# Kernel tuning notes

Hardware: AMD Instinct MI355X
Metric: run time of the kernel (lower is better)

Reference implementation:

```python
import jax, jax.numpy as jnp
import numpy as np
import math

T, R, H, DK = 3, 4, 8, 32   # num_types, num_relations, n_heads, d_k
OUT = H * DK                # out_dim = 256
IN = 256                    # in_dim (== out_dim, required by residual)
B, N = 4, 1024              # batch, max_nodes
LN_EPS = 1e-5


def setup_inputs() -> dict:
    key = jax.random.key(0)
    ks = jax.random.split(key, 12)
    a = math.sqrt(6.0 / (2 * DK))  # xavier_uniform bound for [d_k,d_k]
    w = 0.02
    return {
        "node_features":   jax.random.normal(ks[0], (B, N, IN), jnp.float32),
        "node_types_soft": jax.random.uniform(ks[1], (B, N, T), jnp.float32),
        "adj_matrix_soft": jax.random.uniform(ks[2], (B, N, N), jnp.float32),
        "edge_types_soft": jax.random.uniform(ks[3], (B, N, N, R), jnp.float32),
        "Wq": jax.random.normal(ks[4], (T, IN, OUT), jnp.float32) * w,
        "bq": jnp.zeros((T, OUT), jnp.float32),
        "Wk": jax.random.normal(ks[5], (T, IN, OUT), jnp.float32) * w,
        "bk": jnp.zeros((T, OUT), jnp.float32),
        "Wv": jax.random.normal(ks[6], (T, IN, OUT), jnp.float32) * w,
        "bv": jnp.zeros((T, OUT), jnp.float32),
        "Wa": jax.random.normal(ks[7], (T, OUT, OUT), jnp.float32) * w,
        "ba": jnp.zeros((T, OUT), jnp.float32),
        "rel_pri": jnp.ones((R, H), jnp.float32),
        "rel_att": jax.random.uniform(ks[8], (R, H, DK, DK), jnp.float32, -a, a),
        "rel_msg": jax.random.uniform(ks[9], (R, H, DK, DK), jnp.float32, -a, a),
        "skip": jnp.ones((T,), jnp.float32),
        "ln_gamma": jnp.ones((T, OUT), jnp.float32),
        "ln_beta": jnp.zeros((T, OUT), jnp.float32),
    }


def _single(x, types, adj, erel, Wq, bq, Wk, bk, Wv, bv, Wa, ba,
            rel_pri, rel_att, rel_msg, skip, ln_gamma, ln_beta):
    # x:[N,in], types:[N,T], adj:[N,N], erel:[N,N,R]
    n = x.shape[0]
    sqrt_dk = float(np.sqrt(DK))
    # per-type projections -> [T,N,H,DK]
    Qt = (jnp.einsum('nd,tdo->tno', x, Wq) + bq[:, None, :]).reshape(T, n, H, DK)
    Kt = (jnp.einsum('nd,tdo->tno', x, Wk) + bk[:, None, :]).reshape(T, n, H, DK)
    Vt = (jnp.einsum('nd,tdo->tno', x, Wv) + bv[:, None, :]).reshape(T, n, H, DK)
    # relation-transformed K/V: [T,R,N,H,DK]
    Ksr = jnp.einsum('tnhd,rhde->trnhe', Kt, rel_att)
    Vsr = jnp.einsum('tnhd,rhde->trnhe', Vt, rel_msg)
    # soft-type mixtures (sums over target/source types factor out of the mask)
    Qbar = jnp.einsum('nt,tnhd->nhd', types, Qt)            # target mix
    Kbar = jnp.einsum('nt,trnhd->rnhd', types, Ksr)         # source mix, per relation
    # accumulated (masked, unnormalized) attention logits [N,N,H]
    res_att = jnp.zeros((n, n, H), x.dtype)
    for r in range(R):
        coef = (adj * erel[:, :, r])[:, :, None] * (rel_pri[r] / sqrt_dk)  # [N,N,H]
        res_att = res_att + coef * jnp.einsum('ihd,jhd->ijh', Qbar, Kbar[r])
    # per-target-row softmax over sources (dim j), zeroed if row-sum tiny
    row_sum = res_att.sum(axis=(1, 2))                       # [N]
    attn = jnp.where((row_sum > 1e-6)[:, None, None],
                     jax.nn.softmax(res_att, axis=1), 0.0)
    # aggregated = sum_{s,r,j} attn * masked score * V_{s,r}  (never builds [N,N,H,DK])
    agg = jnp.zeros((n, H, DK), x.dtype)
    for r in range(R):
        coef = (adj * erel[:, :, r])[:, :, None] * (rel_pri[r] / sqrt_dk)
        for s in range(T):
            score = coef * types[None, :, s, None] * jnp.einsum('ihd,jhd->ijh', Qbar, Ksr[s, r])
            agg = agg + jnp.einsum('ijh,ijh,jhd->ihd', attn, score, Vsr[s, r])
    agg = agg.reshape(n, OUT)
    # per-type output head: a_linear(gelu(agg)), gated residual, layernorm, soft-type mix
    g = jax.nn.gelu(agg, approximate=False)
    trans = jnp.einsum('no,tod->tnd', g, Wa) + ba[:, None, :]          # [T,N,OUT]
    alpha = jax.nn.sigmoid(skip)[:, None, None]
    res = trans * alpha + x[None] * (1.0 - alpha)
    mu = res.mean(axis=-1, keepdims=True)
    var = ((res - mu) ** 2).mean(axis=-1, keepdims=True)
    ln = (res - mu) / jnp.sqrt(var + LN_EPS) * ln_gamma[:, None, :] + ln_beta[:, None, :]
    return jnp.einsum('nt,tnd->nd', types, ln)


def reference(node_features, node_types_soft, adj_matrix_soft, edge_types_soft,
              Wq, bq, Wk, bk, Wv, bv, Wa, ba, rel_pri, rel_att, rel_msg,
              skip, ln_gamma, ln_beta):
    f = jax.vmap(_single, in_axes=(0, 0, 0, 0) + (None,) * 14)
    return f(node_features, node_types_soft, adj_matrix_soft, edge_types_soft,
             Wq, bq, Wk, bk, Wv, bv, Wa, ba, rel_pri, rel_att, rel_msg,
             skip, ln_gamma, ln_beta)
```

## Files before the change

kernel.cpp:

```cpp
#include <hip/hip_runtime.h>
#include <math.h>

constexpr int CB = 4, CN = 1024, CT = 3, CR = 4, CH = 8, CDK = 32, COUT = 256;

typedef __attribute__((ext_vector_type(4))) float f32x4;
typedef __attribute__((ext_vector_type(8))) short s16x8;
typedef __attribute__((ext_vector_type(2))) _Float16 f16x2;
typedef __attribute__((ext_vector_type(4))) _Float16 f16x4;
typedef __attribute__((ext_vector_type(8))) _Float16 f16x8;
typedef __attribute__((ext_vector_type(4))) unsigned short u16x4;
typedef __attribute__((ext_vector_type(8))) unsigned short u16x8;

union W4 { f16x4 v4; f16x2 v2[2]; };

__device__ inline unsigned short f2bf(float x) {
    unsigned u = __float_as_uint(x);
    unsigned r = (u + 0x7fffu + ((u >> 16) & 1u)) >> 16;
    return (unsigned short)r;
}
__device__ inline float bf2f(unsigned short b) {
    return __uint_as_float(((unsigned)b) << 16);
}
__device__ inline f16x2 pk2(float a, float b) {
    auto t = __builtin_amdgcn_cvt_pkrtz(a, b);
    f16x2 r;
    __builtin_memcpy(&r, &t, sizeof(r));
    return r;
}

__global__ __launch_bounds__(256) void prep0(
    const float* __restrict__ nf,
    unsigned short* __restrict__ Xh, unsigned short* __restrict__ Xl,
    const float* __restrict__ Wq, const float* __restrict__ Wk,
    const float* __restrict__ Wv, const float* __restrict__ Wa,
    unsigned short* __restrict__ WTh, unsigned short* __restrict__ WTl,
    const float* __restrict__ rel_msg, _Float16* __restrict__ MT,
    float* __restrict__ rs,
    const float* __restrict__ adj, const float* __restrict__ erel,
    float* __restrict__ coefT)
{
    __shared__ float smem[32 * 132];
    const int bx = blockIdx.x, tid = threadIdx.x;
    if (bx < 1024) {
        size_t idx = ((size_t)bx * 256 + tid) * 4;
        f32x4 v = *(const f32x4*)(nf + idx);
        u16x4 hv, lv;
        #pragma unroll
        for (int k = 0; k < 4; ++k) {
            unsigned short hb = f2bf(v[k]);
            hv[k] = hb; lv[k] = f2bf(v[k] - bf2f(hb));
        }
        *(u16x4*)(Xh + idx) = hv;
        *(u16x4*)(Xl + idx) = lv;
    } else if (bx < 1792) {
        int w = bx - 1024;
        int zz = w >> 6; int rem = w & 63;
        int k0 = (rem >> 3) * 32, n0 = (rem & 7) * 32;
        int t = zz % 3;
        const float* W;
        if (zz < 9) { int w3 = zz / 3; W = (w3 == 0 ? Wq : (w3 == 1 ? Wk : Wv)); }
        else W = Wa;
        W += (size_t)t * COUT * COUT;
        {
            int k = tid >> 3, n4 = (tid & 7) * 4;
            f32x4 v = *(const f32x4*)(W + (size_t)(k0 + k) * COUT + n0 + n4);
            smem[(n4 + 0) * 33 + k] = v[0]; smem[(n4 + 1) * 33 + k] = v[1];
            smem[(n4 + 2) * 33 + k] = v[2]; smem[(n4 + 3) * 33 + k] = v[3];
        }
        __syncthreads();
        int n = tid >> 3, k4 = (tid & 7) * 4;
        u16x4 hv, lv;
        #pragma unroll
        for (int j = 0; j < 4; ++j) {
            float x = smem[n * 33 + k4 + j];
            unsigned short hb = f2bf(x);
            hv[j] = hb; lv[j] = f2bf(x - bf2f(hb));
        }
        size_t off = (size_t)zz * COUT * COUT + (size_t)(n0 + n) * COUT + k0 + k4;
        *(u16x4*)(WTh + off) = hv;
        *(u16x4*)(WTl + off) = lv;
    } else if (bx < 1824) {
        int rh = bx - 1792;
        int e = tid >> 3, ep4 = (tid & 7) * 4;
        f16x4 o;
        #pragma unroll
        for (int k = 0; k < 4; ++k)
            o[k] = (_Float16)rel_msg[((size_t)rh * 32 + ep4 + k) * 32 + e];
        *(f16x4*)(MT + ((size_t)rh * 32 + e) * 32 + ep4) = o;
    } else if (bx < 1840) {
        rs[(bx - 1824) * 256 + tid] = 0.f;
    } else {
        int c = bx - 1840;
        int b = c >> 10; int rem = c & 1023;
        int i0 = (rem >> 5) * 32; int j0 = (rem & 31) * 32;
        {
            int ii = tid >> 3, jc = tid & 7;
            size_t arow = ((size_t)b * CN + i0 + ii) * CN + j0;
            f32x4 av = *(const f32x4*)(adj + arow + jc * 4);
            #pragma unroll
            for (int kk = 0; kk < 4; ++kk) {
                int j = jc * 4 + kk;
                f32x4 ev = *(const f32x4*)(erel + (arow + j) * 4);
                float a = av[kk];
                f32x4 cv;
                cv[0] = ev[0] * a; cv[1] = ev[1] * a; cv[2] = ev[2] * a; cv[3] = ev[3] * a;
                *(f32x4*)&smem[j * 132 + ii * 4] = cv;
            }
        }
        __syncthreads();
        {
            int jj = tid >> 3, ic = tid & 7;
            size_t orow = ((size_t)b * CN + j0 + jj) * CN + i0;
            #pragma unroll
            for (int kk = 0; kk < 4; ++kk)
                *(f32x4*)(coefT + (orow + ic * 4 + kk) * 4) =
                    *(const f32x4*)&smem[jj * 132 + (ic * 4 + kk) * 4];
        }
    }
}

__global__ __launch_bounds__(256) void mfma_gemm(
    int mode,
    const unsigned short* __restrict__ Ah, const unsigned short* __restrict__ Al,
    const unsigned short* __restrict__ WTh, const unsigned short* __restrict__ WTl,
    const float* __restrict__ bq, const float* __restrict__ bk,
    const float* __restrict__ bv, const float* __restrict__ ba,
    float* __restrict__ Y0, float* __restrict__ Y1, float* __restrict__ Y2)
{
    int z = blockIdx.z;
    int b, t, widx;
    const float* bias;
    float* Y;
    if (mode == 0) {
        b = z / 9; int r9 = z % 9; int w3 = r9 / 3; t = r9 % 3;
        widx = w3 * 3 + t;
        bias = (w3 == 0 ? bq : (w3 == 1 ? bk : bv)) + t * COUT;
        Y = (w3 == 0 ? Y0 : (w3 == 1 ? Y1 : Y2)) + ((size_t)b * CT + t) * CN * COUT;
    } else {
        b = z / CT; t = z % CT;
        widx = 9 + t;
        bias = ba + t * COUT;
        Y = Y0 + ((size_t)b * CT + t) * CN * COUT;
    }
    const unsigned short* Ahb = Ah + (size_t)b * CN * COUT;
    const unsigned short* Alb = Al + (size_t)b * CN * COUT;
    const unsigned short* Bhb = WTh + (size_t)widx * COUT * COUT;
    const unsigned short* Blb = WTl + (size_t)widx * COUT * COUT;

    const int M0 = blockIdx.x * 128, N0 = blockIdx.y * 128;
    __shared__ unsigned short As[2][128][40];
    __shared__ unsigned short Bs[2][128][40];
    const int tid = threadIdx.x;
    const int wave = tid >> 6, lane = tid & 63;
    const int wm = wave & 1, wn = wave >> 1;
    const int col = lane & 15, quad = lane >> 4;

    f32x4 acc[4][4];
    #pragma unroll
    for (int mt = 0; mt < 4; ++mt)
        #pragma unroll
        for (int nt = 0; nt < 4; ++nt) acc[mt][nt] = (f32x4){0.f, 0.f, 0.f, 0.f};

    for (int kt = 0; kt < COUT; kt += 32) {
        #pragma unroll
        for (int q = 0; q < 2; ++q) {
            int f = q * 256 + tid;
            int m = f >> 2, kc = (f & 3) * 8;
            *(u16x8*)&As[0][m][kc] = *(const u16x8*)(Ahb + (size_t)(M0 + m) * COUT + kt + kc);
            *(u16x8*)&As[1][m][kc] = *(const u16x8*)(Alb + (size_t)(M0 + m) * COUT + kt + kc);
            *(u16x8*)&Bs[0][m][kc] = *(const u16x8*)(Bhb + (size_t)(N0 + m) * COUT + kt + kc);
            *(u16x8*)&Bs[1][m][kc] = *(const u16x8*)(Blb + (size_t)(N0 + m) * COUT + kt + kc);
        }
        __syncthreads();
        s16x8 ah[4], al4[4], bh[4], bl4[4];
        #pragma unroll
        for (int mt = 0; mt < 4; ++mt) {
            ah[mt]  = *(const s16x8*)&As[0][wm * 64 + mt * 16 + col][quad * 8];
            al4[mt] = *(const s16x8*)&As[1][wm * 64 + mt * 16 + col][quad * 8];
        }
        #pragma unroll
        for (int nt = 0; nt < 4; ++nt) {
            bh[nt]  = *(const s16x8*)&Bs[0][wn * 64 + nt * 16 + col][quad * 8];
            bl4[nt] = *(const s16x8*)&Bs[1][wn * 64 + nt * 16 + col][quad * 8];
        }
        #pragma unroll
        for (int mt = 0; mt < 4; ++mt)
            #pragma unroll
            for (int nt = 0; nt < 4; ++nt) {
                acc[mt][nt] = __builtin_amdgcn_mfma_f32_16x16x32_bf16(al4[mt], bh[nt], acc[mt][nt], 0, 0, 0);
                acc[mt][nt] = __builtin_amdgcn_mfma_f32_16x16x32_bf16(ah[mt], bl4[nt], acc[mt][nt], 0, 0, 0);
                acc[mt][nt] = __builtin_amdgcn_mfma_f32_16x16x32_bf16(ah[mt], bh[nt], acc[mt][nt], 0, 0, 0);
            }
        __syncthreads();
    }
    float bb[4];
    #pragma unroll
    for (int nt = 0; nt < 4; ++nt) bb[nt] = bias[N0 + wn * 64 + nt * 16 + col];
    #pragma unroll
    for (int mt = 0; mt < 4; ++mt)
        #pragma unroll
        for (int nt = 0; nt < 4; ++nt) {
            int n = N0 + wn * 64 + nt * 16 + col;
            #pragma unroll
            for (int reg = 0; reg < 4; ++reg) {
                int m = M0 + wm * 64 + mt * 16 + quad * 4 + reg;
                Y[(size_t)m * COUT + n] = acc[mt][nt][reg] + bb[nt];
            }
        }
}

__global__ void mix_qbar(const float* __restrict__ Qt, const float* __restrict__ types,
                         float* __restrict__ Qbar)
{
    int idx = blockIdx.x * 256 + threadIdx.x;
    int bi = idx >> 6;
    int o4 = (idx & 63) * 4;
    int b = bi >> 10;
    const float* tp = types + (size_t)bi * CT;
    float t0 = tp[0], t1 = tp[1], t2 = tp[2];
    size_t nbase = ((size_t)b * CT) * CN * COUT + (size_t)(bi & 1023) * COUT + o4;
    float4 q0 = *(const float4*)(Qt + nbase);
    float4 q1 = *(const float4*)(Qt + nbase + (size_t)CN * COUT);
    float4 q2 = *(const float4*)(Qt + nbase + 2 * (size_t)CN * COUT);
    float4 o;
    o.x = t0 * q0.x + t1 * q1.x + t2 * q2.x;
    o.y = t0 * q0.y + t1 * q1.y + t2 * q2.y;
    o.z = t0 * q0.z + t1 * q1.z + t2 * q2.z;
    o.w = t0 * q0.w + t1 * q1.w + t2 * q2.w;
    *(float4*)(Qbar + (size_t)bi * COUT + o4) = o;
}

__global__ __launch_bounds__(256) void qr3_kernel(const float* __restrict__ Qbar,
                                                  const float* __restrict__ rel_att,
                                                  const float* __restrict__ rel_pri,
                                                  unsigned short* __restrict__ Qrhi,
                                                  unsigned short* __restrict__ Qrlo)
{
    int i0 = blockIdx.x * 8;
    int rh = blockIdx.y; int r = rh >> 3, h = rh & 7;
    int b = blockIdx.z;
    __shared__ float A_s[32][33];
    __shared__ float q_s[8][32];
    int tid = threadIdx.x;
    {
        int f = tid * 4; int d = f >> 5, e = f & 31;
        float4 v = *(const float4*)(rel_att + ((size_t)rh * 32 + d) * 32 + e);
        A_s[d][e] = v.x; A_s[d][e + 1] = v.y; A_s[d][e + 2] = v.z; A_s[d][e + 3] = v.w;
        int ii = tid >> 5, ee = tid & 31;
        q_s[ii][ee] = Qbar[((size_t)b * CN + i0 + ii) * COUT + h * CDK + ee];
    }
    __syncthreads();
    int d = tid & 31, ii = tid >> 5;
    float acc = 0.f;
    #pragma unroll 8
    for (int e = 0; e < 32; ++e) acc += A_s[d][e] * q_s[ii][e];
    const float inv_sqrt = 0.17677669529663687f;
    float v = acc * rel_pri[rh] * inv_sqrt;
    unsigned short hb = f2bf(v);
    float lo = v - bf2f(hb);
    size_t oidx = ((((size_t)b * CR + r) * CH + h) * CN + i0 + ii) * CDK + d;
    Qrhi[oidx] = hb;
    Qrlo[oidx] = f2bf(lo);
}

__global__ __launch_bounds__(256) void prep_kv(
    const float* __restrict__ Kt, const float* __restrict__ Vt,
    const float* __restrict__ types,
    unsigned short* __restrict__ Kbh, unsigned short* __restrict__ Kbl,
    unsigned short* __restrict__ Kty, _Float16* __restrict__ VT)
{
    __shared__ float tile[32][72];
    const int bx = blockIdx.x, tid = threadIdx.x;
    if (bx < 512) {
        int b = bx >> 7, jt = bx & 127;
        int j = jt * 8 + (tid >> 5);
        int c = tid & 31;
        int h = c >> 2, d0 = (c & 3) * 8;
        const float* tp = types + ((size_t)b * CN + j) * CT;
        float kb[8];
        #pragma unroll
        for (int k = 0; k < 8; ++k) kb[k] = 0.f;
        #pragma unroll
        for (int s = 0; s < 3; ++s) {
            float ty = tp[s];
            const float* src = Kt + (((size_t)(b * 3 + s)) * CN + j) * COUT + c * 8;
            f32x4 a0 = *(const f32x4*)(src);
            f32x4 a1 = *(const f32x4*)(src + 4);
            u16x8 kt8;
            #pragma unroll
            for (int k = 0; k < 4; ++k) {
                float v0 = ty * a0[k], v1 = ty * a1[k];
                kt8[k] = f2bf(v0); kt8[4 + k] = f2bf(v1);
                kb[k] += v0; kb[4 + k] += v1;
            }
            *(u16x8*)(Kty + (((size_t)(b * 3 + s) * CH + h) * CN + j) * CDK + d0) = kt8;
        }
        u16x8 hv, lv;
        #pragma unroll
        for (int k = 0; k < 8; ++k) {
            unsigned short hb = f2bf(kb[k]);
            hv[k] = hb; lv[k] = f2bf(kb[k] - bf2f(hb));
        }
        *(u16x8*)(Kbh + (((size_t)b * CH + h) * CN + j) * CDK + d0) = hv;
        *(u16x8*)(Kbl + (((size_t)b * CH + h) * CN + j) * CDK + d0) = lv;
    } else {
        int idx2 = bx - 512;
        int bs = idx2 >> 7; int rem = idx2 & 127;
        int h = rem >> 4; int j0 = (rem & 15) * 64;
        int jj = tid >> 2, e8 = (tid & 3) * 8;
        const float* src = Vt + ((size_t)bs * CN + j0 + jj) * COUT + h * CDK + e8;
        f32x4 v0 = *(const f32x4*)(src);
        f32x4 v1 = *(const f32x4*)(src + 4);
        #pragma unroll
        for (int k = 0; k < 4; ++k) { tile[e8 + k][jj] = v0[k]; tile[e8 + 4 + k][jj] = v1[k]; }
        __syncthreads();
        int e = tid >> 3, jr = (tid & 7) * 8;
        f16x8 o;
        #pragma unroll
        for (int k = 0; k < 8; ++k) o[k] = (_Float16)tile[e][jr + k];
        int jg = j0 + jr;
        int js = jg >> 4, jp = jg & 15;
        *(f16x8*)(VT + ((size_t)(bs * CH + h) * 64 + js) * 512 + e * 16 + jp) = o;
    }
}

__global__ __launch_bounds__(256, 3) void attn5_kernel(
    const unsigned short* __restrict__ Qrhi, const unsigned short* __restrict__ Qrlo,
    const unsigned short* __restrict__ Kbh,  const unsigned short* __restrict__ Kbl,
    const unsigned short* __restrict__ Kty,
    const _Float16* __restrict__ VT,
    const float* __restrict__ coefT,
    float* __restrict__ Upart, float* __restrict__ lbuf, float* __restrict__ rowsum)
{
    const int h = blockIdx.y;
    const int z = blockIdx.z; const int b = z >> 1, part = z & 1;
    const int tid = threadIdx.x;
    const int wave = tid >> 6, lane = tid & 63;
    const int col = lane & 15, quad = lane >> 4;
    const int i = blockIdx.x * 64 + wave * 16 + col;
    const int jbase = part * 512;

    s16x8 qh[4], ql[4];
    #pragma unroll
    for (int r = 0; r < 4; ++r) {
        size_t off = ((((size_t)b * CR + r) * CH + h) * CN + i) * CDK + quad * 8;
        qh[r] = *(const s16x8*)(Qrhi + off);
        ql[r] = *(const s16x8*)(Qrlo + off);
    }

    f32x4 U[4][2];
    #pragma unroll
    for (int r = 0; r < 4; ++r) { U[r][0] = (f32x4){0.f,0.f,0.f,0.f}; U[r][1] = (f32x4){0.f,0.f,0.f,0.f}; }
    float lpart = 0.f, rspart = 0.f;

    const size_t kbbase = (((size_t)b * CH + h) * CN + col) * CDK + quad * 8;
    size_t ktbase[3];
    #pragma unroll
    for (int s = 0; s < 3; ++s)
        ktbase[s] = (((size_t)(b * 3 + s) * CH + h) * CN + col) * CDK + quad * 8;
    const size_t cfrow = ((size_t)b * CN + quad * 4) * CN + i;
    size_t vb[3];
    #pragma unroll
    for (int s = 0; s < 3; ++s)
        vb[s] = ((size_t)((b * 3 + s) * CH + h) * 64) * 512 + col * 16 + quad * 4;

    s16x8 p_bh[2], p_bl[2];
    f32x4 p_cf[2][4];
    f16x4 p_v0[2][3], p_v1[2][3];
    {
        const int j0 = jbase;
        p_bh[0] = *(const s16x8*)(Kbh + kbbase + (size_t)j0 * CDK);
        p_bl[0] = *(const s16x8*)(Kbl + kbbase + (size_t)j0 * CDK);
        #pragma unroll
        for (int reg = 0; reg < 4; ++reg)
            p_cf[0][reg] = *(const f32x4*)(coefT + (cfrow + (size_t)(j0 + reg) * CN) * 4);
        const size_t vo = (size_t)(j0 >> 4) * 512;
        #pragma unroll
        for (int s = 0; s < 3; ++s) {
            p_v0[0][s] = *(const f16x4*)(VT + vb[s] + vo);
            p_v1[0][s] = *(const f16x4*)(VT + vb[s] + vo + 256);
        }
    }

    #pragma unroll 2
    for (int js = 0; js < 32; ++js) {
        const int cur = js & 1, nx = cur ^ 1;
        const int j0 = jbase + js * 16;
        s16x8 kt0 = *(const s16x8*)(Kty + ktbase[0] + (size_t)j0 * CDK);
        s16x8 kt1 = *(const s16x8*)(Kty + ktbase[1] + (size_t)j0 * CDK);
        s16x8 kt2 = *(const s16x8*)(Kty + ktbase[2] + (size_t)j0 * CDK);
        const int jn = jbase + ((js + 1 < 32) ? (js + 1) * 16 : js * 16);
        p_bh[nx] = *(const s16x8*)(Kbh + kbbase + (size_t)jn * CDK);
        p_bl[nx] = *(const s16x8*)(Kbl + kbbase + (size_t)jn * CDK);
        #pragma unroll
        for (int reg = 0; reg < 4; ++reg)
            p_cf[nx][reg] = *(const f32x4*)(coefT + (cfrow + (size_t)(jn + reg) * CN) * 4);
        const size_t von = (size_t)(jn >> 4) * 512;
        #pragma unroll
        for (int s = 0; s < 3; ++s) {
            p_v0[nx][s] = *(const f16x4*)(VT + vb[s] + von);
            p_v1[nx][s] = *(const f16x4*)(VT + vb[s] + von + 256);
        }

        f32x4 Db[4];
        #pragma unroll
        for (int r = 0; r < 4; ++r) {
            f32x4 d = {0.f, 0.f, 0.f, 0.f};
            d = __builtin_amdgcn_mfma_f32_16x16x32_bf16(p_bl[cur], qh[r], d, 0, 0, 0);
            d = __builtin_amdgcn_mfma_f32_16x16x32_bf16(p_bh[cur], ql[r], d, 0, 0, 0);
            d = __builtin_amdgcn_mfma_f32_16x16x32_bf16(p_bh[cur], qh[r], d, 0, 0, 0);
            Db[r] = d;
        }
        float P[4];
        #pragma unroll
        for (int reg = 0; reg < 4; ++reg) {
            float L = p_cf[cur][reg][0] * Db[0][reg] + p_cf[cur][reg][1] * Db[1][reg]
                    + p_cf[cur][reg][2] * Db[2][reg] + p_cf[cur][reg][3] * Db[3][reg];
            rspart += L;
            P[reg] = __expf(L);
            lpart += P[reg];
        }
        f16x2 pA[4], pB[4];
        #pragma unroll
        for (int r = 0; r < 4; ++r) {
            pA[r] = pk2(P[0] * p_cf[cur][0][r], P[1] * p_cf[cur][1][r]);
            pB[r] = pk2(P[2] * p_cf[cur][2][r], P[3] * p_cf[cur][3][r]);
        }
        #pragma unroll
        for (int s = 0; s < 3; ++s) {
            s16x8 kts = (s == 0) ? kt0 : (s == 1) ? kt1 : kt2;
            f32x4 Dp[4];
            #pragma unroll
            for (int r = 0; r < 4; ++r) {
                f32x4 d = {0.f, 0.f, 0.f, 0.f};
                Dp[r] = __builtin_amdgcn_mfma_f32_16x16x32_bf16(kts, qh[r], d, 0, 0, 0);
            }
            f16x4 v0 = p_v0[cur][s];
            f16x4 v1 = p_v1[cur][s];
            #pragma unroll
            for (int r = 0; r < 4; ++r) {
                W4 w;
                w.v2[0] = pA[r] * pk2(Dp[r][0], Dp[r][1]);
                w.v2[1] = pB[r] * pk2(Dp[r][2], Dp[r][3]);
                U[r][0] = __builtin_amdgcn_mfma_f32_16x16x16f16(v0, w.v4, U[r][0], 0, 0, 0);
                U[r][1] = __builtin_amdgcn_mfma_f32_16x16x16f16(v1, w.v4, U[r][1], 0, 0, 0);
            }
        }
    }

    float l = lpart;  l += __shfl_xor(l, 16);  l += __shfl_xor(l, 32);
    float rv = rspart; rv += __shfl_xor(rv, 16); rv += __shfl_xor(rv, 32);
    if (quad == 0) {
        lbuf[(((size_t)part * CB + b) * CH + h) * CN + i] = l;
        atomicAdd(rowsum + (size_t)b * CN + i, rv);
    }
    int itile = blockIdx.x * 4 + wave;
    size_t ub = ((((size_t)(b * CH + h) * 64 + itile) * 2 + part)) * 2048;
    #pragma unroll
    for (int r = 0; r < 4; ++r)
        #pragma unroll
        for (int eh = 0; eh < 2; ++eh)
            *(f32x4*)(Upart + ub + (size_t)(r * 2 + eh) * 256 + lane * 4) = U[r][eh];
}

__global__ __launch_bounds__(256) void merge_gelu(
    const float* __restrict__ Upart, const float* __restrict__ lbuf,
    const _Float16* __restrict__ MT, const float* __restrict__ rowsum,
    unsigned short* __restrict__ Gh, unsigned short* __restrict__ Gl)
{
    const int h = blockIdx.y, b = blockIdx.z;
    const int tid = threadIdx.x;
    const int wave = tid >> 6, lane = tid & 63;
    const int col = lane & 15, quad = lane >> 4;
    const int itile = blockIdx.x * 4 + wave;
    const int i = itile * 16 + col;

    size_t ub = ((size_t)(b * CH + h) * 64 + itile) * 2 * 2048;
    f32x4 U[4][2];
    #pragma unroll
    for (int r = 0; r < 4; ++r)
        #pragma unroll
        for (int eh = 0; eh < 2; ++eh) {
            f32x4 a = *(const f32x4*)(Upart + ub + (size_t)(r * 2 + eh) * 256 + lane * 4);
            f32x4 c = *(const f32x4*)(Upart + ub + 2048 + (size_t)(r * 2 + eh) * 256 + lane * 4);
            U[r][eh] = a + c;
        }
    float l = lbuf[(((size_t)0 * CB + b) * CH + h) * CN + i]
            + lbuf[(((size_t)1 * CB + b) * CH + h) * CN + i];
    float il = 1.f / l;
    f16x4 Uh[4][2];
    #pragma unroll
    for (int r = 0; r < 4; ++r)
        #pragma unroll
        for (int eh = 0; eh < 2; ++eh) {
            Uh[r][eh][0] = (_Float16)(U[r][eh][0] * il);
            Uh[r][eh][1] = (_Float16)(U[r][eh][1] * il);
            Uh[r][eh][2] = (_Float16)(U[r][eh][2] * il);
            Uh[r][eh][3] = (_Float16)(U[r][eh][3] * il);
        }
    float rsv = rowsum[(size_t)b * CN + i];
    bool gate = rsv > 1e-6f;
    const float is2 = 0.70710678118654752f;
    #pragma unroll
    for (int eo = 0; eo < 2; ++eo) {
        f32x4 acc = {0.f, 0.f, 0.f, 0.f};
        #pragma unroll
        for (int r = 0; r < 4; ++r)
            #pragma unroll
            for (int ep = 0; ep < 2; ++ep) {
                f16x4 mt = *(const f16x4*)(MT + ((size_t)(r * 8 + h) * 32 + eo * 16 + col) * 32
                                               + ep * 16 + quad * 4);
                acc = __builtin_amdgcn_mfma_f32_16x16x16f16(mt, Uh[r][ep], acc, 0, 0, 0);
            }
        u16x4 hv, lv;
        #pragma unroll
        for (int k = 0; k < 4; ++k) {
            float x = gate ? acc[k] : 0.f;
            float g = 0.5f * x * (1.f + erff(x * is2));
            unsigned short hb = f2bf(g);
            hv[k] = hb; lv[k] = f2bf(g - bf2f(hb));
        }
        size_t off = ((size_t)b * CN + i) * COUT + h * CDK + eo * 16 + quad * 4;
        *(u16x4*)(Gh + off) = hv;
        *(u16x4*)(Gl + off) = lv;
    }
}

__global__ __launch_bounds__(256) void final_ln2(
    const float* __restrict__ trans, const float* __restrict__ x,
    const float* __restrict__ types, const float* __restrict__ skip,
    const float* __restrict__ gamma, const float* __restrict__ beta,
    float* __restrict__ out)
{
    int wave = threadIdx.x >> 6, lane = threadIdx.x & 63;
    int bi = blockIdx.x * 4 + wave;
    int b = bi >> 10, i = bi & 1023;
    f32x4 xo = *(const f32x4*)(x + (size_t)bi * COUT + lane * 4);
    f32x4 accum = {0.f, 0.f, 0.f, 0.f};
    const float* tp = types + (size_t)bi * CT;
    #pragma unroll 1
    for (int t = 0; t < CT; ++t) {
        float al = 1.f / (1.f + __expf(-skip[t]));
        f32x4 tr = *(const f32x4*)(trans + (((size_t)b * CT + t) * CN + i) * COUT + lane * 4);
        f32x4 res;
        float s = 0.f;
        #pragma unroll
        for (int k = 0; k < 4; ++k) { res[k] = tr[k] * al + xo[k] * (1.f - al); s += res[k]; }
        #pragma unroll
        for (int mk = 1; mk < 64; mk <<= 1) s += __shfl_xor(s, mk);
        float mu = s * (1.f / COUT);
        f32x4 dc; float s2 = 0.f;
        #pragma unroll
        for (int k = 0; k < 4; ++k) { dc[k] = res[k] - mu; s2 += dc[k] * dc[k]; }
        #pragma unroll
        for (int mk = 1; mk < 64; mk <<= 1) s2 += __shfl_xor(s2, mk);
        float inv = rsqrtf(s2 * (1.f / COUT) + 1e-5f);
        f32x4 g = *(const f32x4*)(gamma + (size_t)t * COUT + lane * 4);
        f32x4 be = *(const f32x4*)(beta + (size_t)t * COUT + lane * 4);
        float ty = tp[t];
        #pragma unroll
        for (int k = 0; k < 4; ++k) accum[k] += ty * (dc[k] * inv * g[k] + be[k]);
    }
    *(f32x4*)(out + (size_t)bi * COUT + lane * 4) = accum;
}

extern "C" void kernel_launch(void* const* d_in, const int* in_sizes, int n_in,
                              void* d_out, int out_size, void* d_ws, size_t ws_size,
                              hipStream_t stream)
{
    (void)in_sizes; (void)n_in; (void)out_size; (void)ws_size;
    const float* nf      = (const float*)d_in[0];
    const float* types   = (const float*)d_in[1];
    const float* adj     = (const float*)d_in[2];
    const float* erel    = (const float*)d_in[3];
    const float* Wq      = (const float*)d_in[4];
    const float* bq      = (const float*)d_in[5];
    const float* Wk      = (const float*)d_in[6];
    const float* bk      = (const float*)d_in[7];
    const float* Wv      = (const float*)d_in[8];
    const float* bv      = (const float*)d_in[9];
    const float* Wa      = (const float*)d_in[10];
    const float* ba      = (const float*)d_in[11];
    const float* rel_pri = (const float*)d_in[12];
    const float* rel_att = (const float*)d_in[13];
    const float* rel_msg = (const float*)d_in[14];
    const float* skip    = (const float*)d_in[15];
    const float* gamma   = (const float*)d_in[16];
    const float* beta    = (const float*)d_in[17];
    float* out = (float*)d_out;

    float* ws = (float*)d_ws;
    size_t o = 0;
    float* pool0 = ws + o; o += 3 * (size_t)CB * CT * CN * COUT;
    float* Qt  = pool0;
    float* Ktb = pool0 + (size_t)CB * CT * CN * COUT;
    float* Vtb = pool0 + 2 * (size_t)CB * CT * CN * COUT;
    float* Qbar = ws + o; o += (size_t)CB * CN * COUT;
    float* rsb  = ws + o; o += (size_t)CB * CN;
    float* lbufp = ws + o; o += 2 * (size_t)CB * CH * CN;
    unsigned short* Qrhi = (unsigned short*)(ws + o); o += (size_t)CB * CR * CN * COUT / 2;
    unsigned short* Qrlo = (unsigned short*)(ws + o); o += (size_t)CB * CR * CN * COUT / 2;
    unsigned short* Kbh  = (unsigned short*)(ws + o); o += (size_t)CB * CH * CN * CDK / 2;
    unsigned short* Kbl  = (unsigned short*)(ws + o); o += (size_t)CB * CH * CN * CDK / 2;
    unsigned short* Kty  = (unsigned short*)(ws + o); o += (size_t)CB * CT * CH * CN * CDK / 2;
    _Float16* VTb = (_Float16*)(ws + o);              o += (size_t)CB * CT * CH * CDK * CN / 2;
    _Float16* MTb = (_Float16*)(ws + o);              o += (size_t)CR * CH * CDK * CDK / 2;
    unsigned short* Xh = (unsigned short*)(ws + o);   o += (size_t)CB * CN * COUT / 2;
    unsigned short* Xl = (unsigned short*)(ws + o);   o += (size_t)CB * CN * COUT / 2;
    unsigned short* Gh = (unsigned short*)(ws + o);   o += (size_t)CB * CN * COUT / 2;
    unsigned short* Gl = (unsigned short*)(ws + o);   o += (size_t)CB * CN * COUT / 2;
    unsigned short* WTh = (unsigned short*)(ws + o);  o += (size_t)12 * COUT * COUT / 2;
    unsigned short* WTl = (unsigned short*)(ws + o);  o += (size_t)12 * COUT * COUT / 2;
    float* coefT = ws + o; o += (size_t)CB * CN * CN * CR;
    float* Upart  = pool0;
    float* transb = pool0 + 3 * (size_t)CB * CN * COUT;

    prep0<<<5936, 256, 0, stream>>>(nf, Xh, Xl, Wq, Wk, Wv, Wa, WTh, WTl,
                                    rel_msg, MTb, rsb, adj, erel, coefT);
    mfma_gemm<<<dim3(8, 2, CB * 9), 256, 0, stream>>>(0, Xh, Xl, WTh, WTl,
                                                      bq, bk, bv, ba, Qt, Ktb, Vtb);
    mix_qbar<<<CB * CN * COUT / 4 / 256, 256, 0, stream>>>(Qt, types, Qbar);
    qr3_kernel<<<dim3(CN / 8, CR * CH, CB), 256, 0, stream>>>(Qbar, rel_att, rel_pri, Qrhi, Qrlo);
    prep_kv<<<2048, 256, 0, stream>>>(Ktb, Vtb, types, Kbh, Kbl, Kty, VTb);
    attn5_kernel<<<dim3(16, CH, CB * 2), 256, 0, stream>>>(Qrhi, Qrlo, Kbh, Kbl, Kty, VTb, coefT,
                                                           Upart, lbufp, rsb);
    merge_gelu<<<dim3(16, CH, CB), 256, 0, stream>>>(Upart, lbufp, MTb, rsb, Gh, Gl);
    mfma_gemm<<<dim3(8, 2, CB * CT), 256, 0, stream>>>(1, Gh, Gl, WTh, WTl,
                                                       bq, bk, bv, ba, transb, transb, transb);
    final_ln2<<<CB * CN / 4, 256, 0, stream>>>(transb, nf, types, skip, gamma, beta, out);
}
```

Measured before the change: 423.6 us.

## Split key range across waves within block and reduce attention partials in LDS

The attention kernel now gives each block one 16-row query tile and spreads the 1024 keys across its four waves, instead of splitting keys across two blocks per query tile. Partial U, softmax denominators and row sums are reduced through shared memory, and the rel_msg projection moves into the attention kernel. The separate merge pass over a global partial buffer becomes a simple elementwise GELU/split kernel. The change also drops the register double-buffered prefetch and raises the occupancy hint to 4, which may expose more load latency. It adds an LDS tail in which only one wave does the final reduction and projection.

```diff
diff --git a/kernel.cpp b/kernel.cpp
--- a/kernel.cpp
+++ b/kernel.cpp
@@ -324,21 +324,24 @@
     }
 }
 
-__global__ __launch_bounds__(256, 3) void attn5_kernel(
+__global__ __launch_bounds__(256, 4) void attn6_kernel(
     const unsigned short* __restrict__ Qrhi, const unsigned short* __restrict__ Qrlo,
     const unsigned short* __restrict__ Kbh,  const unsigned short* __restrict__ Kbl,
     const unsigned short* __restrict__ Kty,
     const _Float16* __restrict__ VT,
     const float* __restrict__ coefT,
-    float* __restrict__ Upart, float* __restrict__ lbuf, float* __restrict__ rowsum)
-{
-    const int h = blockIdx.y;
-    const int z = blockIdx.z; const int b = z >> 1, part = z & 1;
+    const _Float16* __restrict__ MT,
+    float* __restrict__ agg, float* __restrict__ rowsum)
+{
+    const int h = blockIdx.y, b = blockIdx.z;
     const int tid = threadIdx.x;
     const int wave = tid >> 6, lane = tid & 63;
     const int col = lane & 15, quad = lane >> 4;
-    const int i = blockIdx.x * 64 + wave * 16 + col;
-    const int jbase = part * 512;
+    const int i0 = blockIdx.x * 16;
+    const int i = i0 + col;
+
+    __shared__ float ldsU[4][64][36];
+    __shared__ float lsh[4][16], rsh[4][16];
 
     s16x8 qh[4], ql[4];
     #pragma unroll
@@ -364,58 +367,40 @@
     for (int s = 0; s < 3; ++s)
         vb[s] = ((size_t)((b * 3 + s) * CH + h) * 64) * 512 + col * 16 + quad * 4;
 
-    s16x8 p_bh[2], p_bl[2];
-    f32x4 p_cf[2][4];
-    f16x4 p_v0[2][3], p_v1[2][3];
-    {
-        const int j0 = jbase;
-        p_bh[0] = *(const s16x8*)(Kbh + kbbase + (size_t)j0 * CDK);
-        p_bl[0] = *(const s16x8*)(Kbl + kbbase + (size_t)j0 * CDK);
-        #pragma unroll
-        for (int reg = 0; reg < 4; ++reg)
-            p_cf[0][reg] = *(const f32x4*)(coefT + (cfrow + (size_t)(j0 + reg) * CN) * 4);
-        const size_t vo = (size_t)(j0 >> 4) * 512;
-        #pragma unroll
-        for (int s = 0; s < 3; ++s) {
-            p_v0[0][s] = *(const f16x4*)(VT + vb[s] + vo);
-            p_v1[0][s] = *(const f16x4*)(VT + vb[s] + vo + 256);
-        }
-    }
-
-    #pragma unroll 2
-    for (int js = 0; js < 32; ++js) {
-        const int cur = js & 1, nx = cur ^ 1;
-        const int j0 = jbase + js * 16;
+    #pragma unroll 1
+    for (int k = 0; k < 16; ++k) {
+        const int j0 = (wave + 4 * k) * 16;
+        s16x8 kbh_ = *(const s16x8*)(Kbh + kbbase + (size_t)j0 * CDK);
+        s16x8 kbl_ = *(const s16x8*)(Kbl + kbbase + (size_t)j0 * CDK);
         s16x8 kt0 = *(const s16x8*)(Kty + ktbase[0] + (size_t)j0 * CDK);
         s16x8 kt1 = *(const s16x8*)(Kty + ktbase[1] + (size_t)j0 * CDK);
         s16x8 kt2 = *(const s16x8*)(Kty + ktbase[2] + (size_t)j0 * CDK);
-        const int jn = jbase + ((js + 1 < 32) ? (js + 1) * 16 : js * 16);
-        p_bh[nx] = *(const s16x8*)(Kbh + kbbase + (size_t)jn * CDK);
-        p_bl[nx] = *(const s16x8*)(Kbl + kbbase + (size_t)jn * CDK);
+        f32x4 cf[4];
         #pragma unroll
         for (int reg = 0; reg < 4; ++reg)
-            p_cf[nx][reg] = *(const f32x4*)(coefT + (cfrow + (size_t)(jn + reg) * CN) * 4);
-        const size_t von = (size_t)(jn >> 4) * 512;
+            cf[reg] = *(const f32x4*)(coefT + (cfrow + (size_t)(j0 + reg) * CN) * 4);
+        const size_t vo = (size_t)(j0 >> 4) * 512;
+        f16x4 v0s[3], v1s[3];
         #pragma unroll
         for (int s = 0; s < 3; ++s) {
-            p_v0[nx][s] = *(const f16x4*)(VT + vb[s] + von);
-            p_v1[nx][s] = *(const f16x4*)(VT + vb[s] + von + 256);
+            v0s[s] = *(const f16x4*)(VT + vb[s] + vo);
+            v1s[s] = *(const f16x4*)(VT + vb[s] + vo + 256);
         }
 
         f32x4 Db[4];
         #pragma unroll
         for (int r = 0; r < 4; ++r) {
             f32x4 d = {0.f, 0.f, 0.f, 0.f};
-            d = __builtin_amdgcn_mfma_f32_16x16x32_bf16(p_bl[cur], qh[r], d, 0, 0, 0);
-            d = __builtin_amdgcn_mfma_f32_16x16x32_bf16(p_bh[cur], ql[r], d, 0, 0, 0);
-            d = __builtin_amdgcn_mfma_f32_16x16x32_bf16(p_bh[cur], qh[r], d, 0, 0, 0);
+            d = __builtin_amdgcn_mfma_f32_16x16x32_bf16(kbl_, qh[r], d, 0, 0, 0);
+            d = __builtin_amdgcn_mfma_f32_16x16x32_bf16(kbh_, ql[r], d, 0, 0, 0);
+            d = __builtin_amdgcn_mfma_f32_16x16x32_bf16(kbh_, qh[r], d, 0, 0, 0);
             Db[r] = d;
         }
         float P[4];
         #pragma unroll
         for (int reg = 0; reg < 4; ++reg) {
-            float L = p_cf[cur][reg][0] * Db[0][reg] + p_cf[cur][reg][1] * Db[1][reg]
-                    + p_cf[cur][reg][2] * Db[2][reg] + p_cf[cur][reg][3] * Db[3][reg];
+            float L = cf[reg][0] * Db[0][reg] + cf[reg][1] * Db[1][reg]
+                    + cf[reg][2] * Db[2][reg] + cf[reg][3] * Db[3][reg];
             rspart += L;
             P[reg] = __expf(L);
             lpart += P[reg];
@@ -423,8 +408,8 @@
         f16x2 pA[4], pB[4];
         #pragma unroll
         for (int r = 0; r < 4; ++r) {
-            pA[r] = pk2(P[0] * p_cf[cur][0][r], P[1] * p_cf[cur][1][r]);
-            pB[r] = pk2(P[2] * p_cf[cur][2][r], P[3] * p_cf[cur][3][r]);
+            pA[r] = pk2(P[0] * cf[0][r], P[1] * cf[1][r]);
+            pB[r] = pk2(P[2] * cf[2][r], P[3] * cf[3][r]);
         }
         #pragma unroll
         for (int s = 0; s < 3; ++s) {
@@ -435,95 +420,86 @@
                 f32x4 d = {0.f, 0.f, 0.f, 0.f};
                 Dp[r] = __builtin_amdgcn_mfma_f32_16x16x32_bf16(kts, qh[r], d, 0, 0, 0);
             }
-            f16x4 v0 = p_v0[cur][s];
-            f16x4 v1 = p_v1[cur][s];
             #pragma unroll
             for (int r = 0; r < 4; ++r) {
                 W4 w;
                 w.v2[0] = pA[r] * pk2(Dp[r][0], Dp[r][1]);
                 w.v2[1] = pB[r] * pk2(Dp[r][2], Dp[r][3]);
-                U[r][0] = __builtin_amdgcn_mfma_f32_16x16x16f16(v0, w.v4, U[r][0], 0, 0, 0);
-                U[r][1] = __builtin_amdgcn_mfma_f32_16x16x16f16(v1, w.v4, U[r][1], 0, 0, 0);
+                U[r][0] = __builtin_amdgcn_mfma_f32_16x16x16f16(v0s[s], w.v4, U[r][0], 0, 0, 0);
+                U[r][1] = __builtin_amdgcn_mfma_f32_16x16x16f16(v1s[s], w.v4, U[r][1], 0, 0, 0);
             }
         }
     }
 
     float l = lpart;  l += __shfl_xor(l, 16);  l += __shfl_xor(l, 32);
     float rv = rspart; rv += __shfl_xor(rv, 16); rv += __shfl_xor(rv, 32);
-    if (quad == 0) {
-        lbuf[(((size_t)part * CB + b) * CH + h) * CN + i] = l;
-        atomicAdd(rowsum + (size_t)b * CN + i, rv);
-    }
-    int itile = blockIdx.x * 4 + wave;
-    size_t ub = ((((size_t)(b * CH + h) * 64 + itile) * 2 + part)) * 2048;
     #pragma unroll
     for (int r = 0; r < 4; ++r)
         #pragma unroll
         for (int eh = 0; eh < 2; ++eh)
-            *(f32x4*)(Upart + ub + (size_t)(r * 2 + eh) * 256 + lane * 4) = U[r][eh];
-}
-
-__global__ __launch_bounds__(256) void merge_gelu(
-    const float* __restrict__ Upart, const float* __restrict__ lbuf,
-    const _Float16* __restrict__ MT, const float* __restrict__ rowsum,
-    unsigned short* __restrict__ Gh, unsigned short* __restrict__ Gl)
-{
-    const int h = blockIdx.y, b = blockIdx.z;
-    const int tid = threadIdx.x;
-    const int wave = tid >> 6, lane = tid & 63;
-    const int col = lane & 15, quad = lane >> 4;
-    const int itile = blockIdx.x * 4 + wave;
-    const int i = itile * 16 + col;
-
-    size_t ub = ((size_t)(b * CH + h) * 64 + itile) * 2 * 2048;
-    f32x4 U[4][2];
-    #pragma unroll
-    for (int r = 0; r < 4; ++r)
-        #pragma unroll
-        for (int eh = 0; eh < 2; ++eh) {
-            f32x4 a = *(const f32x4*)(Upart + ub + (size_t)(r * 2 + eh) * 256 + lane * 4);
-            f32x4 c = *(const f32x4*)(Upart + ub + 2048 + (size_t)(r * 2 + eh) * 256 + lane * 4);
-            U[r][eh] = a + c;
-        }
-    float l = lbuf[(((size_t)0 * CB + b) * CH + h) * CN + i]
-            + lbuf[(((size_t)1 * CB + b) * CH + h) * CN + i];
-    float il = 1.f / l;
-    f16x4 Uh[4][2];
-    #pragma unroll
-    for (int r = 0; r < 4; ++r)
-        #pragma unroll
-        for (int eh = 0; eh < 2; ++eh) {
-            Uh[r][eh][0] = (_Float16)(U[r][eh][0] * il);
-            Uh[r][eh][1] = (_Float16)(U[r][eh][1] * il);
-            Uh[r][eh][2] = (_Float16)(U[r][eh][2] * il);
-            Uh[r][eh][3] = (_Float16)(U[r][eh][3] * il);
-        }
-    float rsv = rowsum[(size_t)b * CN + i];
+            *(f32x4*)&ldsU[wave][lane][(r * 2 + eh) * 4] = U[r][eh];
+    if (quad == 0) { lsh[wave][col] = l; rsh[wave][col] = rv; }
+    __syncthreads();
+
+    if (wave == 0) {
+        f32x4 Us[8];
+        #pragma unroll
+        for (int v = 0; v < 8; ++v) {
+            f32x4 a0 = *(const f32x4*)&ldsU[0][lane][v * 4];
+            f32x4 a1 = *(const f32x4*)&ldsU[1][lane][v * 4];
+            f32x4 a2 = *(const f32x4*)&ldsU[2][lane][v * 4];
+            f32x4 a3 = *(const f32x4*)&ldsU[3][lane][v * 4];
+            Us[v] = (a0 + a1) + (a2 + a3);
+        }
+        float lt = lsh[0][col] + lsh[1][col] + lsh[2][col] + lsh[3][col];
+        float il = 1.f / lt;
+        f16x4 Uh[8];
+        #pragma unroll
+        for (int v = 0; v < 8; ++v) {
+            Uh[v][0] = (_Float16)(Us[v][0] * il);
+            Uh[v][1] = (_Float16)(Us[v][1] * il);
+            Uh[v][2] = (_Float16)(Us[v][2] * il);
+            Uh[v][3] = (_Float16)(Us[v][3] * il);
+        }
+        #pragma unroll
+        for (int eo = 0; eo < 2; ++eo) {
+            f32x4 acc = {0.f, 0.f, 0.f, 0.f};
+            #pragma unroll
+            for (int r = 0; r < 4; ++r)
+                #pragma unroll
+                for (int ep = 0; ep < 2; ++ep) {
+                    f16x4 mt = *(const f16x4*)(MT + ((size_t)(r * 8 + h) * 32 + eo * 16 + col) * 32
+                                                   + ep * 16 + quad * 4);
+                    acc = __builtin_amdgcn_mfma_f32_16x16x16f16(mt, Uh[r * 2 + ep], acc, 0, 0, 0);
+                }
+            *(f32x4*)(agg + ((size_t)b * CN + i) * COUT + h * CDK + eo * 16 + quad * 4) = acc;
+        }
+        if (lane < 16) {
+            float rt = rsh[0][lane] + rsh[1][lane] + rsh[2][lane] + rsh[3][lane];
+            atomicAdd(rowsum + (size_t)b * CN + i0 + lane, rt);
+        }
+    }
+}
+
+__global__ void gelu_split(const float* __restrict__ agg, const float* __restrict__ rowsum,
+                           unsigned short* __restrict__ Gh, unsigned short* __restrict__ Gl)
+{
+    int idx = blockIdx.x * 256 + threadIdx.x;
+    int bi = idx >> 6;
+    float rsv = rowsum[bi];
     bool gate = rsv > 1e-6f;
+    f32x4 v = *(const f32x4*)(agg + (size_t)idx * 4);
     const float is2 = 0.70710678118654752f;
-    #pragma unroll
-    for (int eo = 0; eo < 2; ++eo) {
-        f32x4 acc = {0.f, 0.f, 0.f, 0.f};
-        #pragma unroll
-        for (int r = 0; r < 4; ++r)
-            #pragma unroll
-            for (int ep = 0; ep < 2; ++ep) {
-                f16x4 mt = *(const f16x4*)(MT + ((size_t)(r * 8 + h) * 32 + eo * 16 + col) * 32
-                                               + ep * 16 + quad * 4);
-                acc = __builtin_amdgcn_mfma_f32_16x16x16f16(mt, Uh[r][ep], acc, 0, 0, 0);
-            }
-        u16x4 hv, lv;
-        #pragma unroll
-        for (int k = 0; k < 4; ++k) {
-            float x = gate ? acc[k] : 0.f;
-            float g = 0.5f * x * (1.f + erff(x * is2));
-            unsigned short hb = f2bf(g);
-            hv[k] = hb; lv[k] = f2bf(g - bf2f(hb));
-        }
-        size_t off = ((size_t)b * CN + i) * COUT + h * CDK + eo * 16 + quad * 4;
-        *(u16x4*)(Gh + off) = hv;
-        *(u16x4*)(Gl + off) = lv;
-    }
+    u16x4 hv, lv;
+    #pragma unroll
+    for (int k = 0; k < 4; ++k) {
+        float x = gate ? v[k] : 0.f;
+        float g = 0.5f * x * (1.f + erff(x * is2));
+        unsigned short hb = f2bf(g);
+        hv[k] = hb; lv[k] = f2bf(g - bf2f(hb));
+    }
+    *(u16x4*)(Gh + (size_t)idx * 4) = hv;
+    *(u16x4*)(Gl + (size_t)idx * 4) = lv;
 }
 
 __global__ __launch_bounds__(256) void final_ln2(
@@ -597,7 +573,6 @@
     float* Vtb = pool0 + 2 * (size_t)CB * CT * CN * COUT;
     float* Qbar = ws + o; o += (size_t)CB * CN * COUT;
     float* rsb  = ws + o; o += (size_t)CB * CN;
-    float* lbufp = ws + o; o += 2 * (size_t)CB * CH * CN;
     unsigned short* Qrhi = (unsigned short*)(ws + o); o += (size_t)CB * CR * CN * COUT / 2;
     unsigned short* Qrlo = (unsigned short*)(ws + o); o += (size_t)CB * CR * CN * COUT / 2;
     unsigned short* Kbh  = (unsigned short*)(ws + o); o += (size_t)CB * CH * CN * CDK / 2;
@@ -612,8 +587,8 @@
     unsigned short* WTh = (unsigned short*)(ws + o);  o += (size_t)12 * COUT * COUT / 2;
     unsigned short* WTl = (unsigned short*)(ws + o);  o += (size_t)12 * COUT * COUT / 2;
     float* coefT = ws + o; o += (size_t)CB * CN * CN * CR;
-    float* Upart  = pool0;
-    float* transb = pool0 + 3 * (size_t)CB * CN * COUT;
+    float* aggb   = Qbar;
+    float* transb = pool0;
 
     prep0<<<5936, 256, 0, stream>>>(nf, Xh, Xl, Wq, Wk, Wv, Wa, WTh, WTl,
                                     rel_msg, MTb, rsb, adj, erel, coefT);
@@ -622,9 +597,9 @@
     mix_qbar<<<CB * CN * COUT / 4 / 256, 256, 0, stream>>>(Qt, types, Qbar);
     qr3_kernel<<<dim3(CN / 8, CR * CH, CB), 256, 0, stream>>>(Qbar, rel_att, rel_pri, Qrhi, Qrlo);
     prep_kv<<<2048, 256, 0, stream>>>(Ktb, Vtb, types, Kbh, Kbl, Kty, VTb);
-    attn5_kernel<<<dim3(16, CH, CB * 2), 256, 0, stream>>>(Qrhi, Qrlo, Kbh, Kbl, Kty, VTb, coefT,
-                                                           Upart, lbufp, rsb);
-    merge_gelu<<<dim3(16, CH, CB), 256, 0, stream>>>(Upart, lbufp, MTb, rsb, Gh, Gl);
+    attn6_kernel<<<dim3(64, CH, CB), 256, 0, stream>>>(Qrhi, Qrlo, Kbh, Kbl, Kty, VTb, coefT,
+                                                       MTb, aggb, rsb);
+    gelu_split<<<CB * CN * COUT / 4 / 256, 256, 0, stream>>>(aggb, rsb, Gh, Gl);
     mfma_gemm<<<dim3(8, 2, CB * CT), 256, 0, stream>>>(1, Gh, Gl, WTh, WTl,
                                                        bq, bk, bv, ba, transb, transb, transb);
     final_ln2<<<CB * CN / 4, 256, 0, stream>>>(transb, nf, types, skip, gamma, beta, out);
```

After: 393.8 us. 1.08x faster.
